# Kernel tuning notes

Hardware: AMD Instinct MI355X
Metric: run time of the kernel (lower is better)

The kernel has to match this reference:

```python
import jax, jax.numpy as jnp
import numpy as np

N_NODES = 50000
N_EDGES = 600000
N_REL = 3
VALUE_NUM, TEXT_NUM, FEAT, CLASSES = 16, 768, 128, 2
N_IDX = 10000


def setup_inputs() -> dict:
    key = jax.random.key(0)
    ks = jax.random.split(key, 24)
    s = 0.05
    inp = {
        'value_feature': jax.random.normal(ks[0], (N_NODES, VALUE_NUM), jnp.float32),
        'text_feature': jax.random.normal(ks[1], (N_NODES, TEXT_NUM), jnp.float32),
        'fc1_w': jax.random.normal(ks[2], (VALUE_NUM, FEAT), jnp.float32) * s,
        'fc1_b': jnp.zeros((FEAT,), jnp.float32),
        'fc2_w': jax.random.normal(ks[3], (TEXT_NUM, FEAT), jnp.float32) * s,
        'fc2_b': jnp.zeros((FEAT,), jnp.float32),
        'relu_w': jax.random.normal(ks[4], (2 * FEAT, FEAT), jnp.float32) * s,
        'relu_b': jnp.zeros((FEAT,), jnp.float32),
        'rgcn1_wrel': jax.random.normal(ks[5], (N_REL, FEAT, FEAT), jnp.float32) * s,
        'rgcn1_wroot': jax.random.normal(ks[6], (FEAT, FEAT), jnp.float32) * s,
        'rgcn1_b': jnp.zeros((FEAT,), jnp.float32),
        'rgcn2_wrel': jax.random.normal(ks[7], (N_REL, FEAT, FEAT), jnp.float32) * s,
        'rgcn2_wroot': jax.random.normal(ks[8], (FEAT, FEAT), jnp.float32) * s,
        'rgcn2_b': jnp.zeros((FEAT,), jnp.float32),
        'fc3_w': jax.random.normal(ks[9], (FEAT, CLASSES), jnp.float32) * s,
        'fc3_b': jnp.zeros((CLASSES,), jnp.float32),
        'edge_index': jax.random.randint(ks[10], (2, N_EDGES), 0, N_NODES, jnp.int64 if jax.config.jax_enable_x64 else jnp.int32),
        'edge_type': jax.random.randint(ks[11], (N_EDGES,), 0, N_REL, jnp.int32),
        'idx': jax.random.randint(ks[12], (N_IDX,), 0, N_NODES, jnp.int32),
    }
    return inp


def _rgcn(x, w_rel, w_root, b, src, dst, etype, n_nodes):
    # Per-relation transform: [R, N, D]
    xw = jnp.einsum('nd,rde->rne', x, w_rel)
    msg = xw[etype, src]  # gather per-edge messages [E, D]
    # mean aggregation per (relation, dst) pair (PyG RGCNConv default aggr='mean')
    deg = jnp.zeros((N_REL, n_nodes), x.dtype).at[etype, dst].add(1.0)
    norm = 1.0 / jnp.maximum(deg[etype, dst], 1.0)  # [E]
    agg = jnp.zeros((n_nodes, x.shape[1]), x.dtype).at[dst].add(msg * norm[:, None])
    return agg + x @ w_root + b


def reference(value_feature, text_feature, fc1_w, fc1_b, fc2_w, fc2_b,
              relu_w, relu_b, rgcn1_wrel, rgcn1_wroot, rgcn1_b,
              rgcn2_wrel, rgcn2_wroot, rgcn2_b, fc3_w, fc3_b,
              edge_index, edge_type, idx):
    src, dst = edge_index[0], edge_index[1]
    v = value_feature @ fc1_w + fc1_b
    t = text_feature @ fc2_w + fc2_b
    h = jnp.concatenate([v, t], axis=1)
    h = jax.nn.leaky_relu(h @ relu_w + relu_b, negative_slope=0.01)
    # dropout is identity at eval
    h = _rgcn(h, rgcn1_wrel, rgcn1_wroot, rgcn1_b, src, dst, edge_type, h.shape[0])
    h = _rgcn(h, rgcn2_wrel, rgcn2_wroot, rgcn2_b, src, dst, edge_type, h.shape[0])
    return h[idx] @ fc3_w + fc3_b
```

## Files before the change

### kernel.cpp

```cpp
#include <hip/hip_runtime.h>
#include <hip/hip_bf16.h>

typedef __attribute__((ext_vector_type(8))) short s16x8;
typedef __attribute__((ext_vector_type(4))) float f32x4;
typedef unsigned short u16;
typedef unsigned int u32;

constexpr int NN = 50000;
constexpr int NE = 600000;
constexpr int NIDX = 10000;

__device__ inline u16 f2b(float x) {
    __hip_bfloat16 h = __float2bfloat16(x);
    return *(u16*)&h;
}

__device__ inline s16x8 pack8(float4 a, float4 b) {
    s16x8 r;
    r[0] = (short)f2b(a.x); r[1] = (short)f2b(a.y);
    r[2] = (short)f2b(a.z); r[3] = (short)f2b(a.w);
    r[4] = (short)f2b(b.x); r[5] = (short)f2b(b.y);
    r[6] = (short)f2b(b.z); r[7] = (short)f2b(b.w);
    return r;
}

__device__ inline void gl_lds16(const void* gptr, void* lptr) {
    __builtin_amdgcn_global_load_lds(
        (const __attribute__((address_space(1))) char*)gptr,
        (__attribute__((address_space(3))) char*)lptr, 16, 0, 0);
}

template <int N> __device__ inline void vmwait() {
    asm volatile("s_waitcnt vmcnt(%0)" :: "n"(N) : "memory");
}
__device__ inline void barrier_nodrains() {
    __builtin_amdgcn_sched_barrier(0);
    __builtin_amdgcn_s_barrier();
    __builtin_amdgcn_sched_barrier(0);
}


__global__ void k_setup(const float* __restrict__ vf,
                        const float* __restrict__ fc1w, const float* __restrict__ fc2w,
                        const float* __restrict__ reluw,
                        const float* __restrict__ fc1b, const float* __restrict__ fc2b,
                        const float* __restrict__ relub,
                        const float* __restrict__ w1rel, const float* __restrict__ w1root,
                        const float* __restrict__ w2rel, const float* __restrict__ w2root,
                        const int* __restrict__ ei, const int* __restrict__ et,
                        const int* __restrict__ idx,
                        float* __restrict__ vfp, u16* __restrict__ WTin,
                        float* __restrict__ bcomb, u16* __restrict__ WT1, u16* __restrict__ WT2,
                        int* __restrict__ deg_node, int* __restrict__ deg_rel,
                        int* __restrict__ mark, int* __restrict__ cnt2, int* __restrict__ list) {
    int b = blockIdx.x, t = threadIdx.x;
    if (b < 6250) {
        int i = b * 256 + t;
        int n = i >> 5, c = i & 31;
        vfp[i] = c < 16 ? vf[n * 16 + c] : 0.f;
    } else if (b < 7050) {
        if (t < 128) {
            int k = b - 6250, c = t;
            float s = 0.f;
            if (k < 768) {
                for (int j = 0; j < 128; ++j) s += fc2w[k * 128 + j] * reluw[(128 + j) * 128 + c];
            } else if (k < 784) {
                int kk = k - 768;
                for (int j = 0; j < 128; ++j) s += fc1w[kk * 128 + j] * reluw[j * 128 + c];
            }
            WTin[c * 800 + k] = f2b(s);
        }
    } else if (b == 7050) {
        if (t < 128) {
            int c = t;
            float s = relub[c];
            for (int j = 0; j < 128; ++j) {
                s += fc1b[j] * reluw[j * 128 + c];
                s += fc2b[j] * reluw[(128 + j) * 128 + c];
            }
            bcomb[c] = s;
        }
    } else if (b < 7563) {
        if (t < 128) {
            int s = b - 7051, c = t;
            float v = (s < 384) ? w1rel[(size_t)s * 128 + c] : w1root[(size_t)(s - 384) * 128 + c];
            WT1[c * 512 + s] = f2b(v);
        }
    } else if (b < 8075) {
        if (t < 128) {
            int s = b - 7563, c = t;
            float v = (s < 384) ? w2rel[(size_t)s * 128 + c] : w2root[(size_t)(s - 384) * 128 + c];
            WT2[c * 512 + s] = f2b(v);
        }
    } else if (b < 10419) {
        int e = (b - 8075) * 256 + t;
        if (e < NE) {
            int dst = ei[NE + e];
            int r = et[e];
            atomicAdd(&deg_node[dst], 1);
            atomicAdd(&deg_rel[r * NN + dst], 1);
        }
    } else {
        int i = (b - 10419) * 256 + t;
        if (i < NIDX) {
            int n = idx[i];
            if (atomicExch(&mark[n], 1) == 0) {
                int p = atomicAdd(cnt2, 1);
                list[p] = n;
            }
        }
    }
}


__global__ void k_alloc_norm(const int* __restrict__ deg_node, int* __restrict__ baseoff,
                             int* __restrict__ counter, const int* __restrict__ deg_rel,
                             float* __restrict__ normf) {
    int b = blockIdx.x;
    if (b < 196) {
        int i = b * 256 + threadIdx.x;
        int lane = threadIdx.x & 63;
        int d = (i < NN) ? deg_node[i] : 0;
        int scan = d;
        for (int off = 1; off < 64; off <<= 1) {
            int t = __shfl_up(scan, off, 64);
            if (lane >= off) scan += t;
        }
        int total = __shfl(scan, 63, 64);
        int wbase = 0;
        if (lane == 63) wbase = atomicAdd(counter, total);
        wbase = __shfl(wbase, 63, 64);
        if (i < NN) baseoff[i] = wbase + scan - d;
    } else {
        int i = (b - 196) * 256 + threadIdx.x;
        if (i < 3 * NN) normf[i] = 1.0f / (float)max(deg_rel[i], 1);
    }
}


__global__ __launch_bounds__(64) void k_agg(const u16* __restrict__ x, u16* __restrict__ A,
                                            const int* __restrict__ elist,
                                            const int* __restrict__ baseoff,
                                            const int* __restrict__ deg_node,
                                            const float* __restrict__ normf) {
    int n = blockIdx.x;
    int lane = threadIdx.x;
    float a0x = 0.f, a0y = 0.f, a1x = 0.f, a1y = 0.f, a2x = 0.f, a2y = 0.f;
    int nb = deg_node[n];
    int b0 = baseoff[n];
    for (int i = 0; i < nb; ++i) {
        int p = elist[b0 + i];
        int src = p & 0xFFFFF;
        int r = p >> 20;
        u32 pair = *(const u32*)&x[(size_t)src * 128 + lane * 2];
        float vx = __uint_as_float((pair & 0xFFFFu) << 16);
        float vy = __uint_as_float((pair >> 16) << 16);
        if (r == 0)      { a0x += vx; a0y += vy; }
        else if (r == 1) { a1x += vx; a1y += vy; }
        else             { a2x += vx; a2y += vy; }
    }
    float n0 = normf[n], n1 = normf[NN + n], n2 = normf[2 * NN + n];
    u32* Ao = (u32*)&A[(size_t)n * 384];
    Ao[lane]        = (u32)f2b(a0x * n0) | ((u32)f2b(a0y * n0) << 16);
    Ao[64 + lane]   = (u32)f2b(a1x * n1) | ((u32)f2b(a1y * n1) << 16);
    Ao[128 + lane]  = (u32)f2b(a2x * n2) | ((u32)f2b(a2y * n2) << 16);
}

__global__ __launch_bounds__(64) void k_agg2(const u16* __restrict__ x, u16* __restrict__ A2buf,
                                             const int* __restrict__ elist,
                                             const int* __restrict__ baseoff,
                                             const int* __restrict__ deg_node,
                                             const float* __restrict__ normf,
                                             const int* __restrict__ list,
                                             const int* __restrict__ cnt2) {
    int i = blockIdx.x;
    if (i >= *cnt2) return;
    int n = list[i];
    int lane = threadIdx.x;
    float a0x = 0.f, a0y = 0.f, a1x = 0.f, a1y = 0.f, a2x = 0.f, a2y = 0.f;
    int nb = deg_node[n];
    int b0 = baseoff[n];
    for (int e = 0; e < nb; ++e) {
        int p = elist[b0 + e];
        int src = p & 0xFFFFF;
        int r = p >> 20;
        u32 pair = *(const u32*)&x[(size_t)src * 128 + lane * 2];
        float vx = __uint_as_float((pair & 0xFFFFu) << 16);
        float vy = __uint_as_float((pair >> 16) << 16);
        if (r == 0)      { a0x += vx; a0y += vy; }
        else if (r == 1) { a1x += vx; a1y += vy; }
        else             { a2x += vx; a2y += vy; }
    }
    float n0 = normf[n], n1 = normf[NN + n], n2 = normf[2 * NN + n];
    u32* Ao = (u32*)&A2buf[(size_t)i * 384];
    Ao[lane]        = (u32)f2b(a0x * n0) | ((u32)f2b(a0y * n0) << 16);
    Ao[64 + lane]   = (u32)f2b(a1x * n1) | ((u32)f2b(a1y * n1) << 16);
    Ao[128 + lane]  = (u32)f2b(a2x * n2) | ((u32)f2b(a2y * n2) << 16);
}


template <typename TA, int K1T, int K2T, bool LRELU, bool LIST>
__device__ __forceinline__ void gemm_body(int bid,
                                          const TA* __restrict__ A1, int lda1,
                                          const TA* __restrict__ A2, int lda2,
                                          const u16* __restrict__ WT, int ldwt,
                                          const float* __restrict__ bias,
                                          u16* __restrict__ out, int Nin,
                                          const int* __restrict__ list,
                                          const int* __restrict__ cntp) {
    constexpr int KT = K1T + K2T;
    constexpr int ABYTES = 64 * 32 * (int)sizeof(TA);
    constexpr int TILEB = ABYTES + 8192;
    constexpr int OPW = (sizeof(TA) == 4) ? 4 : 3;
    __shared__ alignas(128) char lds[3][TILEB];

    const int N = LIST ? *cntp : Nin;
    const int m0 = bid * 64;
    if (LIST && m0 >= N) return;

    const int tid = threadIdx.x;
    const int w = tid >> 6, lane = tid & 63;
    const int wr = w >> 1, wc = w & 1;
    const int lq = lane >> 4, lr = lane & 15;

    auto stage = [&](int j) {
        char* base = lds[j % 3];
        int kt = j;
        if constexpr (sizeof(TA) == 4) {
#pragma unroll
            for (int jj = 0; jj < 2; ++jj) {
                int row = w * 16 + jj * 8 + (lane >> 3);
                int s = lane & 7;
                int chunk = s ^ (row & 7);
                int rg = min(m0 + row, N - 1);
                const float* g;
                if (kt < K1T) g = (const float*)A1 + (size_t)rg * lda1 + kt * 32 + chunk * 4;
                else          g = (const float*)A2 + (size_t)rg * lda2 + (kt - K1T) * 32 + chunk * 4;
                gl_lds16(g, base + w * 2048 + jj * 1024);
            }
        } else {
            int row = w * 16 + (lane >> 2);
            int s = lane & 3;
            int chunk = s ^ ((row >> 1) & 3);
            int rg = min(m0 + row, N - 1);
            const u16* g;
            if (kt < K1T) {
                g = (const u16*)A1 + (size_t)rg * lda1 + kt * 32 + chunk * 8;
            } else {
                int node = LIST ? list[rg] : rg;
                g = (const u16*)A2 + (size_t)node * lda2 + (kt - K1T) * 32 + chunk * 8;
            }
            gl_lds16(g, base + w * 1024);
        }
#pragma unroll
        for (int jj = 0; jj < 2; ++jj) {
            int col = w * 32 + jj * 16 + (lane >> 2);
            int s = lane & 3;
            int chunk = s ^ ((col >> 1) & 3);
            const u16* g = WT + (size_t)col * ldwt + kt * 32 + chunk * 8;
            gl_lds16(g, base + ABYTES + w * 2048 + jj * 1024);
        }
    };

    f32x4 acc[2][4] = {};

    auto compute = [&](int j) {
        char* base = lds[j % 3];
        s16x8 af[2];
#pragma unroll
        for (int i = 0; i < 2; ++i) {
            int row = wr * 32 + i * 16 + lr;
            if constexpr (sizeof(TA) == 4) {
                int m = row & 7;
                float4 f0 = *(const float4*)(base + row * 128 + (((2 * lq) ^ m) * 16));
                float4 f1 = *(const float4*)(base + row * 128 + (((2 * lq + 1) ^ m) * 16));
                af[i] = pack8(f0, f1);
            } else {
                int sl = lq ^ ((row >> 1) & 3);
                af[i] = *(const s16x8*)(base + row * 64 + sl * 16);
            }
        }
#pragma unroll
        for (int j4 = 0; j4 < 4; ++j4) {
            int col = wc * 64 + j4 * 16 + lr;
            int sl = lq ^ ((col >> 1) & 3);
            s16x8 bf = *(const s16x8*)(base + ABYTES + col * 64 + sl * 16);
#pragma unroll
            for (int i = 0; i < 2; ++i)
                acc[i][j4] = __builtin_amdgcn_mfma_f32_16x16x32_bf16(af[i], bf, acc[i][j4], 0, 0, 0);
        }
    };

    stage(0); stage(1);
#pragma unroll 1
    for (int j = 0; j < KT - 1; ++j) {
        vmwait<OPW>();
        barrier_nodrains();
        if (j + 2 < KT) stage(j + 2);
        compute(j);
    }
    vmwait<0>();
    barrier_nodrains();
    compute(KT - 1);

#pragma unroll
    for (int i = 0; i < 2; ++i) {
#pragma unroll
        for (int q = 0; q < 4; ++q) {
            int grow = m0 + wr * 32 + i * 16 + lq * 4 + q;
            if (grow < N) {
                int orow = LIST ? list[grow] : grow;
#pragma unroll
                for (int j = 0; j < 4; ++j) {
                    int col = wc * 64 + j * 16 + lr;
                    float v = acc[i][j][q] + bias[col];
                    if (LRELU) v = v > 0.f ? v : 0.01f * v;
                    out[(size_t)orow * 128 + col] = f2b(v);
                }
            }
        }
    }
}


__global__ __launch_bounds__(256) void k_gin_fill(
        const float* __restrict__ A1, int lda1,
        const float* __restrict__ A2, int lda2,
        const u16* __restrict__ WT, int ldwt,
        const float* __restrict__ bias, u16* __restrict__ out, int N,
        const int* __restrict__ ei, const int* __restrict__ et,
        const int* __restrict__ baseoff, int* __restrict__ cursor,
        int* __restrict__ elist) {
    int b = blockIdx.x, t = threadIdx.x;
    if (b < 782) {
        gemm_body<float, 24, 1, true, false>(b, A1, lda1, A2, lda2, WT, ldwt,
                                             bias, out, N, nullptr, nullptr);
    } else {
        int e = (b - 782) * 256 + t;
        if (e < NE) {
            int dst = ei[NE + e];
            int src = ei[e];
            int r = et[e];
            int pos = atomicAdd(&cursor[dst], 1);
            elist[baseoff[dst] + pos] = src | (r << 20);
        }
    }
}

__global__ __launch_bounds__(256) void k_gemm_r1(const u16* __restrict__ A1, int lda1,
                                                 const u16* __restrict__ A2, int lda2,
                                                 const u16* __restrict__ WT, int ldwt,
                                                 const float* __restrict__ bias,
                                                 u16* __restrict__ out, int N) {
    gemm_body<u16, 12, 4, false, false>(blockIdx.x, A1, lda1, A2, lda2, WT, ldwt,
                                        bias, out, N, nullptr, nullptr);
}
__global__ __launch_bounds__(256) void k_gemm_r2(const u16* __restrict__ A1, int lda1,
                                                 const u16* __restrict__ A2, int lda2,
                                                 const u16* __restrict__ WT, int ldwt,
                                                 const float* __restrict__ bias,
                                                 u16* __restrict__ out,
                                                 const int* __restrict__ list,
                                                 const int* __restrict__ cnt2) {
    gemm_body<u16, 12, 4, false, true>(blockIdx.x, A1, lda1, A2, lda2, WT, ldwt,
                                       bias, out, NIDX, list, cnt2);
}


__global__ __launch_bounds__(256) void k_out(const u16* __restrict__ h, const int* __restrict__ idx,
                                             const float* __restrict__ fc3w,
                                             const float* __restrict__ fc3b,
                                             float* __restrict__ out, int M) {
    int w = threadIdx.x >> 6;
    int lane = threadIdx.x & 63;
    int row = blockIdx.x * 4 + w;
    if (row >= M) return;
    int n = idx[row];
    u32 pair = *(const u32*)&h[(size_t)n * 128 + lane * 2];
    float v0 = __uint_as_float((pair & 0xFFFFu) << 16);
    float v1 = __uint_as_float((pair >> 16) << 16);
    float4 wv = *(const float4*)&fc3w[lane * 4];
    float s0 = v0 * wv.x + v1 * wv.z;
    float s1 = v0 * wv.y + v1 * wv.w;
    for (int off = 32; off >= 1; off >>= 1) {
        s0 += __shfl_xor(s0, off, 64);
        s1 += __shfl_xor(s1, off, 64);
    }
    if (lane == 0) {
        out[row * 2] = s0 + fc3b[0];
        out[row * 2 + 1] = s1 + fc3b[1];
    }
}


extern "C" void kernel_launch(void* const* d_in, const int* in_sizes, int n_in,
                              void* d_out, int out_size, void* d_ws, size_t ws_size,
                              hipStream_t stream) {
    const float* vf    = (const float*)d_in[0];
    const float* tf    = (const float*)d_in[1];
    const float* fc1w  = (const float*)d_in[2];
    const float* fc1b  = (const float*)d_in[3];
    const float* fc2w  = (const float*)d_in[4];
    const float* fc2b  = (const float*)d_in[5];
    const float* reluw = (const float*)d_in[6];
    const float* relub = (const float*)d_in[7];
    const float* w1rel = (const float*)d_in[8];
    const float* w1root= (const float*)d_in[9];
    const float* b1    = (const float*)d_in[10];
    const float* w2rel = (const float*)d_in[11];
    const float* w2root= (const float*)d_in[12];
    const float* b2    = (const float*)d_in[13];
    const float* fc3w  = (const float*)d_in[14];
    const float* fc3b  = (const float*)d_in[15];
    const int* ei      = (const int*)d_in[16];
    const int* et      = (const int*)d_in[17];
    const int* idx     = (const int*)d_in[18];
    float* out = (float*)d_out;

    char* W = (char*)d_ws;
    const size_t OFF_WTIN  = 0;
    const size_t OFF_WT1   = 204800;
    const size_t OFF_WT2   = 335872;
    const size_t OFF_BCOMB = 466944;
    const size_t OFF_DEGN  = 467456;
    const size_t OFF_CUR   = 667456;
    const size_t OFF_DEGR  = 867456;
    const size_t OFF_CNT   = 1467456;
    const size_t OFF_CNT2  = 1467460;
    const size_t OFF_MARK  = 1467464;
    const size_t OFF_BASE  = 1667520;
    const size_t OFF_NORM  = 1867520;
    const size_t OFF_ELIST = 2467520;
    const size_t OFF_A     = 4867520;
    const size_t OFF_H0    = 43267520;
    const size_t OFF_H1    = 56067520;
    const size_t OFF_H2    = 68867520;
    const size_t OFF_VFPAD = 81667520;
    const size_t OFF_LIST  = 88067520;
    const size_t OFF_A2    = 88107520;

    u16* WTin   = (u16*)(W + OFF_WTIN);
    u16* WT1    = (u16*)(W + OFF_WT1);
    u16* WT2    = (u16*)(W + OFF_WT2);
    float* bcomb= (float*)(W + OFF_BCOMB);
    int* degn   = (int*)(W + OFF_DEGN);
    int* cur    = (int*)(W + OFF_CUR);
    int* degr   = (int*)(W + OFF_DEGR);
    int* cnt    = (int*)(W + OFF_CNT);
    int* cnt2   = (int*)(W + OFF_CNT2);
    int* mark   = (int*)(W + OFF_MARK);
    int* base   = (int*)(W + OFF_BASE);
    float* normf= (float*)(W + OFF_NORM);
    int* elist  = (int*)(W + OFF_ELIST);
    u16* Abuf   = (u16*)(W + OFF_A);
    u16* h0     = (u16*)(W + OFF_H0);
    u16* h1     = (u16*)(W + OFF_H1);
    u16* h2     = (u16*)(W + OFF_H2);
    float* vfp  = (float*)(W + OFF_VFPAD);
    int* list   = (int*)(W + OFF_LIST);
    u16* A2buf  = (u16*)(W + OFF_A2);

    const int GRID_GEMM = (NN + 63) / 64;
    const int GRID_G2   = (NIDX + 63) / 64;

    hipMemsetAsync(W + OFF_DEGN, 0, 1200008, stream);

    k_setup<<<10459, 256, 0, stream>>>(vf, fc1w, fc2w, reluw, fc1b, fc2b, relub,
                                       w1rel, w1root, w2rel, w2root, ei, et, idx,
                                       vfp, WTin, bcomb, WT1, WT2,
                                       degn, degr, mark, cnt2, list);

    k_alloc_norm<<<782, 256, 0, stream>>>(degn, base, cnt, degr, normf);

    k_gin_fill<<<3126, 256, 0, stream>>>(tf, 768, vfp, 32, WTin, 800, bcomb, h0, NN,
                                         ei, et, base, cur, elist);

    k_agg<<<NN, 64, 0, stream>>>(h0, Abuf, elist, base, degn, normf);
    k_gemm_r1<<<GRID_GEMM, 256, 0, stream>>>(Abuf, 384, h0, 128, WT1, 512, b1, h1, NN);

    k_agg2<<<NIDX, 64, 0, stream>>>(h1, A2buf, elist, base, degn, normf, list, cnt2);
    k_gemm_r2<<<GRID_G2, 256, 0, stream>>>(A2buf, 384, h1, 128, WT2, 512, b2, h2, list, cnt2);

    k_out<<<(NIDX + 3) / 4, 256, 0, stream>>>(h2, idx, fc3w, fc3b, out, NIDX);
}
```

Measured before the change: 229.9 us.

## Vectorize weight fold, drop node-degree atomics, unroll gathers, enlarge RGCN GEMM tile

The fc2/relu weight-folding step now computes four output columns per thread with float4 loads across all 256 threads, so it needs far fewer blocks. The per-node degree atomic is removed and the degree is rebuilt from the three per-relation counts in the scan kernel. The aggregation loop is unrolled by four so several independent row gathers are in flight at once. The RGCN GEMMs use a 128-row tile with a matching vmcnt wait value, which raises reuse per block but halves the grid and increases LDS and register use.

```diff
diff --git a/kernel.cpp b/kernel.cpp
--- a/kernel.cpp
+++ b/kernel.cpp
@@ -51,26 +51,38 @@
                         const int* __restrict__ idx,
                         float* __restrict__ vfp, u16* __restrict__ WTin,
                         float* __restrict__ bcomb, u16* __restrict__ WT1, u16* __restrict__ WT2,
-                        int* __restrict__ deg_node, int* __restrict__ deg_rel,
+                        int* __restrict__ deg_rel,
                         int* __restrict__ mark, int* __restrict__ cnt2, int* __restrict__ list) {
     int b = blockIdx.x, t = threadIdx.x;
     if (b < 6250) {
         int i = b * 256 + t;
         int n = i >> 5, c = i & 31;
         vfp[i] = c < 16 ? vf[n * 16 + c] : 0.f;
-    } else if (b < 7050) {
-        if (t < 128) {
-            int k = b - 6250, c = t;
-            float s = 0.f;
-            if (k < 768) {
-                for (int j = 0; j < 128; ++j) s += fc2w[k * 128 + j] * reluw[(128 + j) * 128 + c];
-            } else if (k < 784) {
-                int kk = k - 768;
-                for (int j = 0; j < 128; ++j) s += fc1w[kk * 128 + j] * reluw[j * 128 + c];
-            }
-            WTin[c * 800 + k] = f2b(s);
-        }
-    } else if (b == 7050) {
+    } else if (b < 6350) {
+        int k = (b - 6250) * 8 + (t >> 5);
+        int c0 = (t & 31) * 4;
+        float4 s = {0.f, 0.f, 0.f, 0.f};
+        if (k < 768) {
+#pragma unroll 4
+            for (int j = 0; j < 128; ++j) {
+                float fw = fc2w[k * 128 + j];
+                float4 rw = *(const float4*)&reluw[(128 + j) * 128 + c0];
+                s.x += fw * rw.x; s.y += fw * rw.y; s.z += fw * rw.z; s.w += fw * rw.w;
+            }
+        } else if (k < 784) {
+            int kk = k - 768;
+#pragma unroll 4
+            for (int j = 0; j < 128; ++j) {
+                float fw = fc1w[kk * 128 + j];
+                float4 rw = *(const float4*)&reluw[j * 128 + c0];
+                s.x += fw * rw.x; s.y += fw * rw.y; s.z += fw * rw.z; s.w += fw * rw.w;
+            }
+        }
+        WTin[(c0 + 0) * 800 + k] = f2b(s.x);
+        WTin[(c0 + 1) * 800 + k] = f2b(s.y);
+        WTin[(c0 + 2) * 800 + k] = f2b(s.z);
+        WTin[(c0 + 3) * 800 + k] = f2b(s.w);
+    } else if (b == 6350) {
         if (t < 128) {
             int c = t;
             float s = relub[c];
@@ -80,28 +92,27 @@
             }
             bcomb[c] = s;
         }
-    } else if (b < 7563) {
+    } else if (b < 6863) {
         if (t < 128) {
-            int s = b - 7051, c = t;
+            int s = b - 6351, c = t;
             float v = (s < 384) ? w1rel[(size_t)s * 128 + c] : w1root[(size_t)(s - 384) * 128 + c];
             WT1[c * 512 + s] = f2b(v);
         }
-    } else if (b < 8075) {
+    } else if (b < 7375) {
         if (t < 128) {
-            int s = b - 7563, c = t;
+            int s = b - 6863, c = t;
             float v = (s < 384) ? w2rel[(size_t)s * 128 + c] : w2root[(size_t)(s - 384) * 128 + c];
             WT2[c * 512 + s] = f2b(v);
         }
-    } else if (b < 10419) {
-        int e = (b - 8075) * 256 + t;
+    } else if (b < 9719) {
+        int e = (b - 7375) * 256 + t;
         if (e < NE) {
             int dst = ei[NE + e];
             int r = et[e];
-            atomicAdd(&deg_node[dst], 1);
             atomicAdd(&deg_rel[r * NN + dst], 1);
         }
     } else {
-        int i = (b - 10419) * 256 + t;
+        int i = (b - 9719) * 256 + t;
         if (i < NIDX) {
             int n = idx[i];
             if (atomicExch(&mark[n], 1) == 0) {
@@ -113,14 +124,15 @@
 }
 
 
-__global__ void k_alloc_norm(const int* __restrict__ deg_node, int* __restrict__ baseoff,
+__global__ void k_alloc_norm(int* __restrict__ deg_node, int* __restrict__ baseoff,
                              int* __restrict__ counter, const int* __restrict__ deg_rel,
                              float* __restrict__ normf) {
     int b = blockIdx.x;
     if (b < 196) {
         int i = b * 256 + threadIdx.x;
         int lane = threadIdx.x & 63;
-        int d = (i < NN) ? deg_node[i] : 0;
+        int d = 0;
+        if (i < NN) d = deg_rel[i] + deg_rel[NN + i] + deg_rel[2 * NN + i];
         int scan = d;
         for (int off = 1; off < 64; off <<= 1) {
             int t = __shfl_up(scan, off, 64);
@@ -130,40 +142,59 @@
         int wbase = 0;
         if (lane == 63) wbase = atomicAdd(counter, total);
         wbase = __shfl(wbase, 63, 64);
-        if (i < NN) baseoff[i] = wbase + scan - d;
+        if (i < NN) { baseoff[i] = wbase + scan - d; deg_node[i] = d; }
     } else {
         int i = (b - 196) * 256 + threadIdx.x;
         if (i < 3 * NN) normf[i] = 1.0f / (float)max(deg_rel[i], 1);
     }
 }
 
+
+template <bool LIST>
+__device__ __forceinline__ void agg_body(int outrow, int n, int lane,
+                                         const u16* __restrict__ x, u16* __restrict__ A,
+                                         const int* __restrict__ elist,
+                                         const int* __restrict__ baseoff,
+                                         const int* __restrict__ deg_node,
+                                         const float* __restrict__ normf) {
+    float a0x = 0.f, a0y = 0.f, a1x = 0.f, a1y = 0.f, a2x = 0.f, a2y = 0.f;
+    int nb = deg_node[n];
+    int b0 = baseoff[n];
+    auto ACC = [&](u32 pair, int r) {
+        float vx = __uint_as_float((pair & 0xFFFFu) << 16);
+        float vy = __uint_as_float((pair >> 16) << 16);
+        if (r == 0)      { a0x += vx; a0y += vy; }
+        else if (r == 1) { a1x += vx; a1y += vy; }
+        else             { a2x += vx; a2y += vy; }
+    };
+    int i = 0;
+    for (; i + 4 <= nb; i += 4) {
+        int p0 = elist[b0 + i], p1 = elist[b0 + i + 1];
+        int p2 = elist[b0 + i + 2], p3 = elist[b0 + i + 3];
+        u32 q0 = *(const u32*)&x[(size_t)(p0 & 0xFFFFF) * 128 + lane * 2];
+        u32 q1 = *(const u32*)&x[(size_t)(p1 & 0xFFFFF) * 128 + lane * 2];
+        u32 q2 = *(const u32*)&x[(size_t)(p2 & 0xFFFFF) * 128 + lane * 2];
+        u32 q3 = *(const u32*)&x[(size_t)(p3 & 0xFFFFF) * 128 + lane * 2];
+        ACC(q0, p0 >> 20); ACC(q1, p1 >> 20); ACC(q2, p2 >> 20); ACC(q3, p3 >> 20);
+    }
+    for (; i < nb; ++i) {
+        int p = elist[b0 + i];
+        u32 q = *(const u32*)&x[(size_t)(p & 0xFFFFF) * 128 + lane * 2];
+        ACC(q, p >> 20);
+    }
+    float n0 = normf[n], n1 = normf[NN + n], n2 = normf[2 * NN + n];
+    u32* Ao = (u32*)&A[(size_t)outrow * 384];
+    Ao[lane]        = (u32)f2b(a0x * n0) | ((u32)f2b(a0y * n0) << 16);
+    Ao[64 + lane]   = (u32)f2b(a1x * n1) | ((u32)f2b(a1y * n1) << 16);
+    Ao[128 + lane]  = (u32)f2b(a2x * n2) | ((u32)f2b(a2y * n2) << 16);
+}
 
 __global__ __launch_bounds__(64) void k_agg(const u16* __restrict__ x, u16* __restrict__ A,
                                             const int* __restrict__ elist,
                                             const int* __restrict__ baseoff,
                                             const int* __restrict__ deg_node,
                                             const float* __restrict__ normf) {
-    int n = blockIdx.x;
-    int lane = threadIdx.x;
-    float a0x = 0.f, a0y = 0.f, a1x = 0.f, a1y = 0.f, a2x = 0.f, a2y = 0.f;
-    int nb = deg_node[n];
-    int b0 = baseoff[n];
-    for (int i = 0; i < nb; ++i) {
-        int p = elist[b0 + i];
-        int src = p & 0xFFFFF;
-        int r = p >> 20;
-        u32 pair = *(const u32*)&x[(size_t)src * 128 + lane * 2];
-        float vx = __uint_as_float((pair & 0xFFFFu) << 16);
-        float vy = __uint_as_float((pair >> 16) << 16);
-        if (r == 0)      { a0x += vx; a0y += vy; }
-        else if (r == 1) { a1x += vx; a1y += vy; }
-        else             { a2x += vx; a2y += vy; }
-    }
-    float n0 = normf[n], n1 = normf[NN + n], n2 = normf[2 * NN + n];
-    u32* Ao = (u32*)&A[(size_t)n * 384];
-    Ao[lane]        = (u32)f2b(a0x * n0) | ((u32)f2b(a0y * n0) << 16);
-    Ao[64 + lane]   = (u32)f2b(a1x * n1) | ((u32)f2b(a1y * n1) << 16);
-    Ao[128 + lane]  = (u32)f2b(a2x * n2) | ((u32)f2b(a2y * n2) << 16);
+    agg_body<false>(blockIdx.x, blockIdx.x, threadIdx.x, x, A, elist, baseoff, deg_node, normf);
 }
 
 __global__ __launch_bounds__(64) void k_agg2(const u16* __restrict__ x, u16* __restrict__ A2buf,
@@ -175,31 +206,11 @@
                                              const int* __restrict__ cnt2) {
     int i = blockIdx.x;
     if (i >= *cnt2) return;
-    int n = list[i];
-    int lane = threadIdx.x;
-    float a0x = 0.f, a0y = 0.f, a1x = 0.f, a1y = 0.f, a2x = 0.f, a2y = 0.f;
-    int nb = deg_node[n];
-    int b0 = baseoff[n];
-    for (int e = 0; e < nb; ++e) {
-        int p = elist[b0 + e];
-        int src = p & 0xFFFFF;
-        int r = p >> 20;
-        u32 pair = *(const u32*)&x[(size_t)src * 128 + lane * 2];
-        float vx = __uint_as_float((pair & 0xFFFFu) << 16);
-        float vy = __uint_as_float((pair >> 16) << 16);
-        if (r == 0)      { a0x += vx; a0y += vy; }
-        else if (r == 1) { a1x += vx; a1y += vy; }
-        else             { a2x += vx; a2y += vy; }
-    }
-    float n0 = normf[n], n1 = normf[NN + n], n2 = normf[2 * NN + n];
-    u32* Ao = (u32*)&A2buf[(size_t)i * 384];
-    Ao[lane]        = (u32)f2b(a0x * n0) | ((u32)f2b(a0y * n0) << 16);
-    Ao[64 + lane]   = (u32)f2b(a1x * n1) | ((u32)f2b(a1y * n1) << 16);
-    Ao[128 + lane]  = (u32)f2b(a2x * n2) | ((u32)f2b(a2y * n2) << 16);
-}
-
-
-template <typename TA, int K1T, int K2T, bool LRELU, bool LIST>
+    agg_body<true>(i, list[i], threadIdx.x, x, A2buf, elist, baseoff, deg_node, normf);
+}
+
+
+template <typename TA, int BM, int K1T, int K2T, bool LRELU, bool LIST>
 __device__ __forceinline__ void gemm_body(int bid,
                                           const TA* __restrict__ A1, int lda1,
                                           const TA* __restrict__ A2, int lda2,
@@ -209,13 +220,17 @@
                                           const int* __restrict__ list,
                                           const int* __restrict__ cntp) {
     constexpr int KT = K1T + K2T;
-    constexpr int ABYTES = 64 * 32 * (int)sizeof(TA);
+    constexpr int MI = BM / 32;
+    constexpr int AJJ = BM / 64;
+    constexpr int ABYTES = BM * 32 * (int)sizeof(TA);
     constexpr int TILEB = ABYTES + 8192;
-    constexpr int OPW = (sizeof(TA) == 4) ? 4 : 3;
+    constexpr int OPW = (sizeof(TA) == 4) ? 6 : (AJJ + 2);
+    constexpr int OPW_F32 = 4;
+    constexpr int OPW_EFF = (sizeof(TA) == 4) ? OPW_F32 : OPW;
     __shared__ alignas(128) char lds[3][TILEB];
 
     const int N = LIST ? *cntp : Nin;
-    const int m0 = bid * 64;
+    const int m0 = bid * BM;
     if (LIST && m0 >= N) return;
 
     const int tid = threadIdx.x;
@@ -239,18 +254,21 @@
                 gl_lds16(g, base + w * 2048 + jj * 1024);
             }
         } else {
-            int row = w * 16 + (lane >> 2);
-            int s = lane & 3;
-            int chunk = s ^ ((row >> 1) & 3);
-            int rg = min(m0 + row, N - 1);
-            const u16* g;
-            if (kt < K1T) {
-                g = (const u16*)A1 + (size_t)rg * lda1 + kt * 32 + chunk * 8;
-            } else {
-                int node = LIST ? list[rg] : rg;
-                g = (const u16*)A2 + (size_t)node * lda2 + (kt - K1T) * 32 + chunk * 8;
-            }
-            gl_lds16(g, base + w * 1024);
+#pragma unroll
+            for (int jj = 0; jj < AJJ; ++jj) {
+                int row = w * (16 * AJJ) + jj * 16 + (lane >> 2);
+                int s = lane & 3;
+                int chunk = s ^ ((row >> 1) & 3);
+                int rg = min(m0 + row, N - 1);
+                const u16* g;
+                if (kt < K1T) {
+                    g = (const u16*)A1 + (size_t)rg * lda1 + kt * 32 + chunk * 8;
+                } else {
+                    int node = LIST ? list[rg] : rg;
+                    g = (const u16*)A2 + (size_t)node * lda2 + (kt - K1T) * 32 + chunk * 8;
+                }
+                gl_lds16(g, base + w * (1024 * AJJ) + jj * 1024);
+            }
         }
 #pragma unroll
         for (int jj = 0; jj < 2; ++jj) {
@@ -262,14 +280,14 @@
         }
     };
 
-    f32x4 acc[2][4] = {};
+    f32x4 acc[MI][4] = {};
 
     auto compute = [&](int j) {
         char* base = lds[j % 3];
-        s16x8 af[2];
-#pragma unroll
-        for (int i = 0; i < 2; ++i) {
-            int row = wr * 32 + i * 16 + lr;
+        s16x8 af[MI];
+#pragma unroll
+        for (int i = 0; i < MI; ++i) {
+            int row = wr * (BM / 2) + i * 16 + lr;
             if constexpr (sizeof(TA) == 4) {
                 int m = row & 7;
                 float4 f0 = *(const float4*)(base + row * 128 + (((2 * lq) ^ m) * 16));
@@ -286,7 +304,7 @@
             int sl = lq ^ ((col >> 1) & 3);
             s16x8 bf = *(const s16x8*)(base + ABYTES + col * 64 + sl * 16);
 #pragma unroll
-            for (int i = 0; i < 2; ++i)
+            for (int i = 0; i < MI; ++i)
                 acc[i][j4] = __builtin_amdgcn_mfma_f32_16x16x32_bf16(af[i], bf, acc[i][j4], 0, 0, 0);
         }
     };
@@ -294,7 +312,7 @@
     stage(0); stage(1);
 #pragma unroll 1
     for (int j = 0; j < KT - 1; ++j) {
-        vmwait<OPW>();
+        vmwait<OPW_EFF>();
         barrier_nodrains();
         if (j + 2 < KT) stage(j + 2);
         compute(j);
@@ -304,10 +322,10 @@
     compute(KT - 1);
 
 #pragma unroll
-    for (int i = 0; i < 2; ++i) {
+    for (int i = 0; i < MI; ++i) {
 #pragma unroll
         for (int q = 0; q < 4; ++q) {
-            int grow = m0 + wr * 32 + i * 16 + lq * 4 + q;
+            int grow = m0 + wr * (BM / 2) + i * 16 + lq * 4 + q;
             if (grow < N) {
                 int orow = LIST ? list[grow] : grow;
 #pragma unroll
@@ -333,8 +351,8 @@
         int* __restrict__ elist) {
     int b = blockIdx.x, t = threadIdx.x;
     if (b < 782) {
-        gemm_body<float, 24, 1, true, false>(b, A1, lda1, A2, lda2, WT, ldwt,
-                                             bias, out, N, nullptr, nullptr);
+        gemm_body<float, 64, 24, 1, true, false>(b, A1, lda1, A2, lda2, WT, ldwt,
+                                                 bias, out, N, nullptr, nullptr);
     } else {
         int e = (b - 782) * 256 + t;
         if (e < NE) {
@@ -352,8 +370,8 @@
                                                  const u16* __restrict__ WT, int ldwt,
                                                  const float* __restrict__ bias,
                                                  u16* __restrict__ out, int N) {
-    gemm_body<u16, 12, 4, false, false>(blockIdx.x, A1, lda1, A2, lda2, WT, ldwt,
-                                        bias, out, N, nullptr, nullptr);
+    gemm_body<u16, 128, 12, 4, false, false>(blockIdx.x, A1, lda1, A2, lda2, WT, ldwt,
+                                             bias, out, N, nullptr, nullptr);
 }
 __global__ __launch_bounds__(256) void k_gemm_r2(const u16* __restrict__ A1, int lda1,
                                                  const u16* __restrict__ A2, int lda2,
@@ -362,8 +380,8 @@
                                                  u16* __restrict__ out,
                                                  const int* __restrict__ list,
                                                  const int* __restrict__ cnt2) {
-    gemm_body<u16, 12, 4, false, true>(blockIdx.x, A1, lda1, A2, lda2, WT, ldwt,
-                                       bias, out, NIDX, list, cnt2);
+    gemm_body<u16, 128, 12, 4, false, true>(blockIdx.x, A1, lda1, A2, lda2, WT, ldwt,
+                                            bias, out, NIDX, list, cnt2);
 }
 
 
@@ -460,15 +478,15 @@
     int* list   = (int*)(W + OFF_LIST);
     u16* A2buf  = (u16*)(W + OFF_A2);
 
-    const int GRID_GEMM = (NN + 63) / 64;
-    const int GRID_G2   = (NIDX + 63) / 64;
+    const int GRID_R1 = (NN + 127) / 128;
+    const int GRID_R2 = (NIDX + 127) / 128;
 
     hipMemsetAsync(W + OFF_DEGN, 0, 1200008, stream);
 
-    k_setup<<<10459, 256, 0, stream>>>(vf, fc1w, fc2w, reluw, fc1b, fc2b, relub,
-                                       w1rel, w1root, w2rel, w2root, ei, et, idx,
-                                       vfp, WTin, bcomb, WT1, WT2,
-                                       degn, degr, mark, cnt2, list);
+    k_setup<<<9759, 256, 0, stream>>>(vf, fc1w, fc2w, reluw, fc1b, fc2b, relub,
+                                      w1rel, w1root, w2rel, w2root, ei, et, idx,
+                                      vfp, WTin, bcomb, WT1, WT2,
+                                      degr, mark, cnt2, list);
 
     k_alloc_norm<<<782, 256, 0, stream>>>(degn, base, cnt, degr, normf);
 
@@ -476,10 +494,10 @@
                                          ei, et, base, cur, elist);
 
     k_agg<<<NN, 64, 0, stream>>>(h0, Abuf, elist, base, degn, normf);
-    k_gemm_r1<<<GRID_GEMM, 256, 0, stream>>>(Abuf, 384, h0, 128, WT1, 512, b1, h1, NN);
+    k_gemm_r1<<<GRID_R1, 256, 0, stream>>>(Abuf, 384, h0, 128, WT1, 512, b1, h1, NN);
 
     k_agg2<<<NIDX, 64, 0, stream>>>(h1, A2buf, elist, base, degn, normf, list, cnt2);
-    k_gemm_r2<<<GRID_G2, 256, 0, stream>>>(A2buf, 384, h1, 128, WT2, 512, b2, h2, list, cnt2);
+    k_gemm_r2<<<GRID_R2, 256, 0, stream>>>(A2buf, 384, h1, 128, WT2, 512, b2, h2, list, cnt2);
 
     k_out<<<(NIDX + 3) / 4, 256, 0, stream>>>(h2, idx, fc3w, fc3b, out, NIDX);
 }
```

Measured after the change: 301.4 us. +31.1%, slower.
